# Optimization experiments

Measured on AMD Instinct MI355X. Metric: run time of the kernel, lower is better.

Reference implementation:

```python
import jax, jax.numpy as jnp
import numpy as np

N_NODES = 50000
N_GRAPHS = 500
E_SPARSE = 800000
E_DENSE = 3200000
IN_DIM = 128
HID = 128          # nb_hidden
OUT = HID // 2     # per-branch GATConv output
N_LAYERS = 3
NEG_SLOPE = 0.2    # PyG GATConv default


def setup_inputs() -> dict:
    key = jax.random.key(0)
    ks = jax.random.split(key, 10)
    x = jax.random.normal(ks[0], (N_NODES, IN_DIM), dtype=jnp.float32)
    edge_index = jax.random.randint(ks[1], (2, E_SPARSE), 0, N_NODES, dtype=jnp.int32)
    dense_edge_idx = jax.random.randint(ks[2], (2, E_DENSE), 0, N_NODES, dtype=jnp.int32)
    batch = jnp.sort(jax.random.randint(ks[3], (N_NODES,), 0, N_GRAPHS, dtype=jnp.int32))
    # One weight set per layer (source code aliases layersB = layersA, so both
    # branches share weights). All layers have in_dim = 128 -> out = 64.
    lin_w = jax.random.normal(ks[4], (N_LAYERS, HID, OUT), dtype=jnp.float32) * 0.1
    att_src = jax.random.normal(ks[5], (N_LAYERS, OUT), dtype=jnp.float32) * 0.1
    att_dst = jax.random.normal(ks[6], (N_LAYERS, OUT), dtype=jnp.float32) * 0.1
    bias = jnp.zeros((N_LAYERS, OUT), dtype=jnp.float32)
    final_w = jax.random.normal(ks[7], (HID, 1), dtype=jnp.float32) * 0.1
    final_b = jnp.zeros((1,), dtype=jnp.float32)
    return {"x": x, "edge_index": edge_index, "dense_edge_idx": dense_edge_idx,
            "batch": batch, "lin_w": lin_w, "att_src": att_src,
            "att_dst": att_dst, "bias": bias, "final_w": final_w,
            "final_b": final_b}


def _with_self_loops(edge_index, n):
    loop = jnp.arange(n, dtype=edge_index.dtype)
    src = jnp.concatenate([edge_index[0], loop])
    dst = jnp.concatenate([edge_index[1], loop])
    return src, dst


def _gat(x, src, dst, W, a_s, a_d, b):
    """PyG GATConv, heads=1: gather, LeakyReLU attention, segment softmax over
    incoming edges of each dst node, scatter-add aggregation."""
    n = x.shape[0]
    h = x @ W                      # [N, OUT]
    s_src = h @ a_s                # [N] per-node source score
    s_dst = h @ a_d                # [N] per-node dest score
    e = jax.nn.leaky_relu(s_src[src] + s_dst[dst], NEG_SLOPE)  # [E]
    m = jax.ops.segment_max(e, dst, num_segments=n)
    p = jnp.exp(e - m[dst])
    z = jax.ops.segment_sum(p, dst, num_segments=n)
    alpha = p / z[dst]             # [E] softmax over neighbors of dst
    out = jax.ops.segment_sum(alpha[:, None] * h[src], dst, num_segments=n)
    return out + b


def reference(x, edge_index, dense_edge_idx, batch, lin_w, att_src, att_dst,
              bias, final_w, final_b):
    n = x.shape[0]
    srcA, dstA = _with_self_loops(edge_index, n)
    srcB, dstB = _with_self_loops(dense_edge_idx, n)
    for l in range(N_LAYERS):
        xA = _gat(x, srcA, dstA, lin_w[l], att_src[l], att_dst[l], bias[l])
        xB = _gat(x, srcB, dstB, lin_w[l], att_src[l], att_dst[l], bias[l])
        x = jax.nn.relu(jnp.concatenate([xA, xB], axis=1))
    g = jax.ops.segment_sum(x, batch, num_segments=N_GRAPHS)  # global_add_pool
    y = (g @ final_w + final_b).squeeze()
    return y
```

## Files before the change

### kernel.cpp

```cpp
#include <hip/hip_runtime.h>
#include <hip/hip_fp16.h>

#define N_NODES 50000
#define N_GRAPHS 500
#define E_SPARSE 800000
#define E_DENSE 3200000
#define IN_DIM 128
#define HID 128
#define OUT_D 64
#define N_LAYERS 3
#define NEG_SLOPE 0.2f

#define BUCKET_SHIFT 7
#define BUCKET_N 128
#define NBUCK 391
#define NTD 256
#define NTS 64
#define TS_D 12500
#define TS_S 12500
#define MD (NBUCK * NTD)
#define MATN (NBUCK * (NTD + NTS))
#define NT 32
typedef unsigned int u32;
typedef unsigned short u16;
typedef _Float16 h16x8 __attribute__((ext_vector_type(8)));


__global__ __launch_bounds__(256) void tile_count_all(
    const int* __restrict__ dstD, const int* __restrict__ dstS,
    int* __restrict__ mat) {
    __shared__ int hc[NBUCK];
    int t = threadIdx.x;
    int tile = blockIdx.x;
    for (int i = t; i < NBUCK; i += 256) hc[i] = 0;
    __syncthreads();
    if (tile < NTD) {
        int beg = tile * TS_D, end = min(E_DENSE, beg + TS_D);
        for (int i = beg + t; i < end; i += 256)
            atomicAdd(&hc[dstD[i] >> BUCKET_SHIFT], 1);
        __syncthreads();
        for (int i = t; i < NBUCK; i += 256) mat[i * NTD + tile] = hc[i];
    } else {
        int st = tile - NTD;
        int beg = st * TS_S, end = min(E_SPARSE, beg + TS_S);
        for (int i = beg + t; i < end; i += 256)
            atomicAdd(&hc[dstS[i] >> BUCKET_SHIFT], 1);
        __syncthreads();
        for (int i = t; i < NBUCK; i += 256) mat[MD + i * NTS + st] = hc[i];
    }
}

__global__ void scan_lvl0(const int* __restrict__ cnt, int n,
                          int* __restrict__ out, int* __restrict__ bsum) {
    __shared__ int sm[512];
    int t = threadIdx.x;
    int base = blockIdx.x * 2048 + t * 4;
    int v0 = (base + 0 < n) ? cnt[base + 0] : 0;
    int v1 = (base + 1 < n) ? cnt[base + 1] : 0;
    int v2 = (base + 2 < n) ? cnt[base + 2] : 0;
    int v3 = (base + 3 < n) ? cnt[base + 3] : 0;
    int s = v0 + v1 + v2 + v3;
    sm[t] = s;
    __syncthreads();
    for (int off = 1; off < 512; off <<= 1) {
        int a = (t >= off) ? sm[t - off] : 0;
        __syncthreads();
        sm[t] += a;
        __syncthreads();
    }
    int excl = sm[t] - s;
    if (base + 0 < n) out[base + 0] = excl;
    if (base + 1 < n) out[base + 1] = excl + v0;
    if (base + 2 < n) out[base + 2] = excl + v0 + v1;
    if (base + 3 < n) out[base + 3] = excl + v0 + v1 + v2;
    if (t == 511) bsum[blockIdx.x] = sm[511];
}

__global__ void scan_lvl1(const int* __restrict__ bsum, int nb,
                          int* __restrict__ bsumx) {
    __shared__ int sm[256];
    int t = threadIdx.x;
    int v = (t < nb) ? bsum[t] : 0;
    sm[t] = v;
    __syncthreads();
    for (int off = 1; off < 256; off <<= 1) {
        int a = (t >= off) ? sm[t - off] : 0;
        __syncthreads();
        sm[t] += a;
        __syncthreads();
    }
    if (t < nb) bsumx[t] = sm[t] - v;
}

__global__ void scan_add(int* __restrict__ out, int n, const int* __restrict__ bsumx,
                         int Etot) {
    int i = blockIdx.x * blockDim.x + threadIdx.x;
    if (i < n) out[i] += bsumx[i >> 11];
    if (i == 0) out[n] = Etot;
}

__global__ __launch_bounds__(256) void tile_scatter_all(
    const int* __restrict__ srcD, const int* __restrict__ dstD,
    const int* __restrict__ srcS, const int* __restrict__ dstS,
    const int* __restrict__ matx, u32* __restrict__ pairs) {
    __shared__ int cur[NBUCK];
    int t = threadIdx.x;
    int tile = blockIdx.x;
    const int* src;
    const int* dst;
    int beg, end;
    if (tile < NTD) {
        for (int i = t; i < NBUCK; i += 256) cur[i] = matx[i * NTD + tile];
        src = srcD; dst = dstD;
        beg = tile * TS_D; end = min(E_DENSE, beg + TS_D);
    } else {
        int st = tile - NTD;
        for (int i = t; i < NBUCK; i += 256) cur[i] = matx[MD + i * NTS + st];
        src = srcS; dst = dstS;
        beg = st * TS_S; end = min(E_SPARSE, beg + TS_S);
    }
    __syncthreads();
    for (int i = beg + t; i < end; i += 256) {
        int d = dst[i];
        int pos = atomicAdd(&cur[d >> BUCKET_SHIFT], 1);
        pairs[pos] = (u32)src[i] | ((u32)(d & (BUCKET_N - 1)) << 16);
    }
}

__global__ __launch_bounds__(256) void bucket_to_csr_all(
    const u32* __restrict__ pairs, const int* __restrict__ matx,
    int* __restrict__ rowD, u16* __restrict__ csrcD,
    int* __restrict__ rowS, u16* __restrict__ csrcS) {
    int bid = blockIdx.x;
    int t = threadIdx.x;
    int b, beg, end, base;
    int* rowptr;
    u16* csrc;
    if (bid < NBUCK) {
        b = bid;
        beg = matx[b * NTD];
        end = matx[(b + 1) * NTD];
        base = 0; rowptr = rowD; csrc = csrcD;
    } else {
        b = bid - NBUCK;
        beg = matx[MD + b * NTS];
        end = matx[MD + (b + 1) * NTS];
        base = E_DENSE; rowptr = rowS; csrc = csrcS;
    }
    __shared__ int lcnt[BUCKET_N];
    __shared__ int lofs[BUCKET_N];
    if (t < BUCKET_N) lcnt[t] = 0;
    __syncthreads();
    for (int k = beg + t; k < end; k += 256)
        atomicAdd(&lcnt[(pairs[k] >> 16) & (BUCKET_N - 1)], 1);
    __syncthreads();
    if (t < BUCKET_N) lofs[t] = lcnt[t];
    __syncthreads();
    for (int off = 1; off < BUCKET_N; off <<= 1) {
        int a = (t < BUCKET_N && t >= off) ? lofs[t - off] : 0;
        __syncthreads();
        if (t < BUCKET_N) lofs[t] += a;
        __syncthreads();
    }
    int node = (b << BUCKET_SHIFT) + t;
    int lbeg = beg - base;
    if (t < BUCKET_N) {
        int excl = lofs[t] - lcnt[t];
        if (node < N_NODES) rowptr[node] = lbeg + excl;
        lcnt[t] = excl;
    }
    if (b == NBUCK - 1 && t == 0)
        rowptr[N_NODES] = (base == 0) ? E_DENSE : E_SPARSE;
    __syncthreads();
    for (int k = beg + t; k < end; k += 256) {
        u32 pr = pairs[k];
        int dl = (pr >> 16) & (BUCKET_N - 1);
        int pos = atomicAdd(&lcnt[dl], 1);
        csrc[lbeg + pos] = (u16)(pr & 0xffffu);
    }
}


__global__ __launch_bounds__(256) void node_mm2(
    const float* __restrict__ x, const float* __restrict__ W,
    const float* __restrict__ a_s, const float* __restrict__ a_d,
    __half* __restrict__ h, float* __restrict__ s_src, float* __restrict__ s_dst) {
    __shared__ float Wl[IN_DIM * OUT_D];
    __shared__ float4 Xl4[NT * 33];
    int t = threadIdx.x;
    int nbase = blockIdx.x * NT;

    const float4* W4 = (const float4*)W;
    float4* Wl4 = (float4*)Wl;
#pragma unroll
    for (int i = 0; i < 8; ++i) Wl4[t + 256 * i] = W4[t + 256 * i];

    int nrows = min(NT, N_NODES - nbase);
    const float4* X4 = (const float4*)(x + (size_t)nbase * IN_DIM);
    for (int i = t; i < nrows * 32; i += 256)
        Xl4[(i >> 5) * 33 + (i & 31)] = X4[i];
    __syncthreads();

    int wv = t >> 6, l = t & 63;
    int c4 = l & 15;
    int np = l >> 4;
    int n0 = wv * 8 + np * 2, n1 = n0 + 1;
    const float* Xl = (const float*)Xl4;
    const float4* Wr = (const float4*)Wl;

    float4 A0 = make_float4(0.f, 0.f, 0.f, 0.f);
    float4 A1 = make_float4(0.f, 0.f, 0.f, 0.f);
#pragma unroll 4
    for (int k = 0; k < IN_DIM; ++k) {
        float4 w4 = Wr[k * 16 + c4];
        float x0 = Xl[n0 * 132 + k];
        float x1 = Xl[n1 * 132 + k];
        A0.x += x0 * w4.x; A0.y += x0 * w4.y; A0.z += x0 * w4.z; A0.w += x0 * w4.w;
        A1.x += x1 * w4.x; A1.y += x1 * w4.y; A1.z += x1 * w4.z; A1.w += x1 * w4.w;
    }
    int gn0 = nbase + n0, gn1 = nbase + n1;
    if (gn0 < N_NODES) {
        __half2 v0 = __floats2half2_rn(A0.x, A0.y);
        __half2 v1 = __floats2half2_rn(A0.z, A0.w);
        float2 pk;
        pk.x = *(float*)&v0; pk.y = *(float*)&v1;
        ((float2*)(h + (size_t)gn0 * OUT_D))[c4] = pk;
    }
    if (gn1 < N_NODES) {
        __half2 v0 = __floats2half2_rn(A1.x, A1.y);
        __half2 v1 = __floats2half2_rn(A1.z, A1.w);
        float2 pk;
        pk.x = *(float*)&v0; pk.y = *(float*)&v1;
        ((float2*)(h + (size_t)gn1 * OUT_D))[c4] = pk;
    }

    float4 as4 = ((const float4*)a_s)[c4];
    float4 ad4 = ((const float4*)a_d)[c4];
    float ps0 = A0.x * as4.x + A0.y * as4.y + A0.z * as4.z + A0.w * as4.w;
    float pd0 = A0.x * ad4.x + A0.y * ad4.y + A0.z * ad4.z + A0.w * ad4.w;
    float ps1 = A1.x * as4.x + A1.y * as4.y + A1.z * as4.z + A1.w * as4.w;
    float pd1 = A1.x * ad4.x + A1.y * ad4.y + A1.z * ad4.z + A1.w * ad4.w;
#pragma unroll
    for (int off = 1; off < 16; off <<= 1) {
        ps0 += __shfl_xor(ps0, off); pd0 += __shfl_xor(pd0, off);
        ps1 += __shfl_xor(ps1, off); pd1 += __shfl_xor(pd1, off);
    }
    if (c4 == 0) {
        if (gn0 < N_NODES) { s_src[gn0] = ps0; s_dst[gn0] = pd0; }
        if (gn1 < N_NODES) { s_src[gn1] = ps1; s_dst[gn1] = pd1; }
    }
}

__device__ __forceinline__ void accv(float4& a0, float4& a1, float p,
                                     const h16x8& r) {
    a0.x = fmaf((float)r[0], p, a0.x);
    a0.y = fmaf((float)r[1], p, a0.y);
    a0.z = fmaf((float)r[2], p, a0.z);
    a0.w = fmaf((float)r[3], p, a0.w);
    a1.x = fmaf((float)r[4], p, a1.x);
    a1.y = fmaf((float)r[5], p, a1.y);
    a1.z = fmaf((float)r[6], p, a1.z);
    a1.w = fmaf((float)r[7], p, a1.w);
}

__device__ __forceinline__ float lrelu(float e) {
    return fmaxf(e, NEG_SLOPE * e);
}

__global__ __launch_bounds__(256, 8) void gat_aggr3(
    const int* __restrict__ rowS, const u16* __restrict__ csrcS,
    const int* __restrict__ rowD, const u16* __restrict__ csrcD,
    const float* __restrict__ s_src, const float* __restrict__ s_dst,
    const __half* __restrict__ h, const float* __restrict__ bias,
    float* __restrict__ xnext, int nblk) {
    int bid = blockIdx.x;
    const int* rowptr;
    const u16* csrc;
    int col_off;
    if (bid < nblk) { rowptr = rowS; csrc = csrcS; col_off = 0; }
    else { bid -= nblk; rowptr = rowD; csrc = csrcD; col_off = OUT_D; }

    int lane = threadIdx.x & 63;
    int wid = threadIdx.x >> 6;
    int grp = lane >> 3;
    int sub = lane & 7;
    int node = bid * 32 + wid * 8 + grp;
    bool valid = node < N_NODES;

    int beg = 0, end = 0;
    if (valid) { beg = rowptr[node]; end = rowptr[node + 1]; }
    float sd = valid ? s_dst[node] : 0.f;

    const char* hb = (const char*)h;
    u32 subo = (u32)sub * 16u;

    float4 a0 = make_float4(0.f, 0.f, 0.f, 0.f);
    float4 a1 = make_float4(0.f, 0.f, 0.f, 0.f);
    float z = 0.f;

    int k = beg;
    for (; k + 1 < end; k += 2) {
        u32 s0 = csrc[k], s1 = csrc[k + 1];
        h16x8 r0 = *(const h16x8*)(hb + (s0 * 128u + subo));
        h16x8 r1 = *(const h16x8*)(hb + (s1 * 128u + subo));
        float e0 = s_src[s0] + sd;
        float e1 = s_src[s1] + sd;
        float p0 = __expf(lrelu(e0));
        float p1 = __expf(lrelu(e1));
        z += p0 + p1;
        accv(a0, a1, p0, r0);
        accv(a0, a1, p1, r1);
    }
    if (k < end) {
        u32 s0 = csrc[k];
        h16x8 r0 = *(const h16x8*)(hb + (s0 * 128u + subo));
        float e0 = s_src[s0] + sd;
        float p0 = __expf(lrelu(e0));
        z += p0;
        accv(a0, a1, p0, r0);
    }
    if (valid) {
        h16x8 r0 = *(const h16x8*)(hb + ((u32)node * 128u + subo));
        float e0 = s_src[node] + sd;
        float p0 = __expf(lrelu(e0));
        z += p0;
        accv(a0, a1, p0, r0);

        float inv = 1.f / z;
        const float4* b4 = (const float4*)bias;
        float4 b0 = b4[sub * 2], b1 = b4[sub * 2 + 1];
        float4 o0, o1;
        o0.x = a0.x * inv + b0.x; o0.y = a0.y * inv + b0.y;
        o0.z = a0.z * inv + b0.z; o0.w = a0.w * inv + b0.w;
        o1.x = a1.x * inv + b1.x; o1.y = a1.y * inv + b1.y;
        o1.z = a1.z * inv + b1.z; o1.w = a1.w * inv + b1.w;
        o0.x = fmaxf(o0.x, 0.f); o0.y = fmaxf(o0.y, 0.f);
        o0.z = fmaxf(o0.z, 0.f); o0.w = fmaxf(o0.w, 0.f);
        o1.x = fmaxf(o1.x, 0.f); o1.y = fmaxf(o1.y, 0.f);
        o1.z = fmaxf(o1.z, 0.f); o1.w = fmaxf(o1.w, 0.f);
        float4* outp = (float4*)(xnext + (size_t)node * HID + col_off);
        outp[sub * 2] = o0;
        outp[sub * 2 + 1] = o1;
    }
}

__global__ __launch_bounds__(128) void pool_final(
    const float* __restrict__ x, const int* __restrict__ batch,
    const float* __restrict__ fw, const float* __restrict__ fb,
    float* __restrict__ y) {
    int b = blockIdx.x;
    int t = threadIdx.x;
    __shared__ int sbeg, send;
    if (t == 0) {
        int lo = 0, hi = N_NODES;
        while (lo < hi) { int mid = (lo + hi) >> 1; if (batch[mid] < b) lo = mid + 1; else hi = mid; }
        sbeg = lo;
        hi = N_NODES;
        while (lo < hi) { int mid = (lo + hi) >> 1; if (batch[mid] < b + 1) lo = mid + 1; else hi = mid; }
        send = lo;
    }
    __syncthreads();
    float acc = 0.f;
    for (int n = sbeg; n < send; ++n) acc += x[(size_t)n * HID + t];
    __shared__ float sm[HID];
    sm[t] = acc * fw[t];
    __syncthreads();
    for (int off = 64; off > 0; off >>= 1) {
        if (t < off) sm[t] += sm[t + off];
        __syncthreads();
    }
    if (t == 0) y[b] = sm[0] + fb[0];
}

extern "C" void kernel_launch(void* const* d_in, const int* in_sizes, int n_in,
                              void* d_out, int out_size, void* d_ws, size_t ws_size,
                              hipStream_t stream) {
    const float* x_in    = (const float*)d_in[0];
    const int*   ei      = (const int*)d_in[1];
    const int*   di      = (const int*)d_in[2];
    const int*   batch   = (const int*)d_in[3];
    const float* lin_w   = (const float*)d_in[4];
    const float* att_src = (const float*)d_in[5];
    const float* att_dst = (const float*)d_in[6];
    const float* bias    = (const float*)d_in[7];
    const float* fw      = (const float*)d_in[8];
    const float* fb      = (const float*)d_in[9];
    float* y = (float*)d_out;

    char* wsb = (char*)d_ws;
    size_t off = 0;
    auto alloc_b = [&](size_t bytes) { void* p = (void*)(wsb + off);
                                       off += (bytes + 15) & ~(size_t)15; return p; };

    float* xbuf0 = (float*)alloc_b((size_t)N_NODES * HID * 4);
    float* xbuf1 = (float*)alloc_b((size_t)N_NODES * HID * 4);
    __half* h    = (__half*)alloc_b((size_t)N_NODES * OUT_D * 2);
    float* s_src = (float*)alloc_b(N_NODES * 4);
    float* s_dst = (float*)alloc_b(N_NODES * 4);
    int* mat     = (int*)alloc_b((size_t)MATN * 4);
    int* matx    = (int*)alloc_b(((size_t)MATN + 1) * 4);
    int* bsum    = (int*)alloc_b(256 * 4);
    int* bsumx   = (int*)alloc_b(256 * 4);
    int* rowS    = (int*)alloc_b((N_NODES + 1) * 4);
    int* rowD    = (int*)alloc_b((N_NODES + 1) * 4);
    u16* csrcS   = (u16*)alloc_b((size_t)E_SPARSE * 2);
    u16* csrcD   = (u16*)alloc_b((size_t)E_DENSE * 2);
    u32* pairs   = (u32*)xbuf1;

    const int* srcD = di;
    const int* dstD = di + E_DENSE;
    const int* srcS = ei;
    const int* dstS = ei + E_SPARSE;

    const int SCAN_BLKS = (MATN + 2047) / 2048;

    tile_count_all<<<NTD + NTS, 256, 0, stream>>>(dstD, dstS, mat);
    scan_lvl0<<<SCAN_BLKS, 512, 0, stream>>>(mat, MATN, matx, bsum);
    scan_lvl1<<<1, 256, 0, stream>>>(bsum, SCAN_BLKS, bsumx);
    scan_add<<<(MATN + 256) / 256, 256, 0, stream>>>(matx, MATN, bsumx,
                                                     E_DENSE + E_SPARSE);
    tile_scatter_all<<<NTD + NTS, 256, 0, stream>>>(srcD, dstD, srcS, dstS,
                                                    matx, pairs);
    bucket_to_csr_all<<<2 * NBUCK, 256, 0, stream>>>(pairs, matx, rowD, csrcD,
                                                     rowS, csrcS);

    const float* cur = x_in;
    float* bufs[3] = {xbuf1, xbuf0, xbuf1};
    const int nblk = (N_NODES + 31) / 32;
    const int mm_grid = (N_NODES + NT - 1) / NT;
    for (int l = 0; l < N_LAYERS; ++l) {
        node_mm2<<<mm_grid, 256, 0, stream>>>(cur, lin_w + (size_t)l * HID * OUT_D,
                                              att_src + l * OUT_D, att_dst + l * OUT_D,
                                              h, s_src, s_dst);
        float* xn = bufs[l];
        gat_aggr3<<<2 * nblk, 256, 0, stream>>>(rowS, csrcS, rowD, csrcD,
                                                s_src, s_dst, h,
                                                bias + l * OUT_D, xn, nblk);
        cur = xn;
    }

    pool_final<<<N_GRAPHS, 128, 0, stream>>>(cur, batch, fw, fb, y);
}
```

Baseline: 511.4 us.

## Split feature gather into column halves with separate softmax-normalizer pass

```diff
diff --git a/kernel.cpp b/kernel.cpp
--- a/kernel.cpp
+++ b/kernel.cpp
@@ -8,6 +8,7 @@
 #define IN_DIM 128
 #define HID 128
 #define OUT_D 64
+#define OUT_H 32
 #define N_LAYERS 3
 #define NEG_SLOPE 0.2f
 
@@ -184,7 +185,8 @@
 __global__ __launch_bounds__(256) void node_mm2(
     const float* __restrict__ x, const float* __restrict__ W,
     const float* __restrict__ a_s, const float* __restrict__ a_d,
-    __half* __restrict__ h, float* __restrict__ s_src, float* __restrict__ s_dst) {
+    __half* __restrict__ h_lo, __half* __restrict__ h_hi,
+    float* __restrict__ s_src, float* __restrict__ s_dst) {
     __shared__ float Wl[IN_DIM * OUT_D];
     __shared__ float4 Xl4[NT * 33];
     int t = threadIdx.x;
@@ -219,19 +221,21 @@
         A1.x += x1 * w4.x; A1.y += x1 * w4.y; A1.z += x1 * w4.z; A1.w += x1 * w4.w;
     }
     int gn0 = nbase + n0, gn1 = nbase + n1;
+    __half* hdst = (c4 < 8) ? h_lo : h_hi;
+    int c4h = c4 & 7;
     if (gn0 < N_NODES) {
         __half2 v0 = __floats2half2_rn(A0.x, A0.y);
         __half2 v1 = __floats2half2_rn(A0.z, A0.w);
         float2 pk;
         pk.x = *(float*)&v0; pk.y = *(float*)&v1;
-        ((float2*)(h + (size_t)gn0 * OUT_D))[c4] = pk;
+        ((float2*)(hdst + (size_t)gn0 * OUT_H))[c4h] = pk;
     }
     if (gn1 < N_NODES) {
         __half2 v0 = __floats2half2_rn(A1.x, A1.y);
         __half2 v1 = __floats2half2_rn(A1.z, A1.w);
         float2 pk;
         pk.x = *(float*)&v0; pk.y = *(float*)&v1;
-        ((float2*)(h + (size_t)gn1 * OUT_D))[c4] = pk;
+        ((float2*)(hdst + (size_t)gn1 * OUT_H))[c4h] = pk;
     }
 
     float4 as4 = ((const float4*)a_s)[c4];
@@ -267,67 +271,101 @@
     return fmaxf(e, NEG_SLOPE * e);
 }
 
-__global__ __launch_bounds__(256, 8) void gat_aggr3(
+__global__ __launch_bounds__(256, 8) void gat_score(
     const int* __restrict__ rowS, const u16* __restrict__ csrcS,
     const int* __restrict__ rowD, const u16* __restrict__ csrcD,
     const float* __restrict__ s_src, const float* __restrict__ s_dst,
-    const __half* __restrict__ h, const float* __restrict__ bias,
-    float* __restrict__ xnext, int nblk) {
+    float* __restrict__ zinvS, float* __restrict__ zinvD, int ngrid) {
     int bid = blockIdx.x;
     const int* rowptr;
     const u16* csrc;
+    float* zinv;
+    if (bid < ngrid) { rowptr = rowS; csrc = csrcS; zinv = zinvS; }
+    else { bid -= ngrid; rowptr = rowD; csrc = csrcD; zinv = zinvD; }
+
+    int wid = threadIdx.x >> 6;
+    int lane = threadIdx.x & 63;
+    int node = bid * 4 + wid;
+    if (node >= N_NODES) return;
+
+    int beg = rowptr[node];
+    int end = rowptr[node + 1];
+    float sd = s_dst[node];
+
+    float z = 0.f;
+    for (int k = beg + lane; k < end; k += 64) {
+        u32 idx = csrc[k];
+        z += __expf(lrelu(s_src[idx] + sd));
+    }
+#pragma unroll
+    for (int off = 1; off <= 32; off <<= 1) z += __shfl_xor(z, off);
+    z += __expf(lrelu(s_src[node] + sd));
+    if (lane == 0) zinv[node] = 1.f / z;
+}
+
+__global__ __launch_bounds__(256, 8) void gat_gath(
+    const int* __restrict__ rowS, const u16* __restrict__ csrcS,
+    const float* __restrict__ zinvS,
+    const int* __restrict__ rowD, const u16* __restrict__ csrcD,
+    const float* __restrict__ zinvD,
+    const float* __restrict__ s_src, const float* __restrict__ s_dst,
+    const __half* __restrict__ hhalf, const float* __restrict__ biasH,
+    float* __restrict__ xnext, int ngrid, int halfoff) {
+    int bid = blockIdx.x;
+    const int* rowptr;
+    const u16* csrc;
+    const float* zinv;
     int col_off;
-    if (bid < nblk) { rowptr = rowS; csrc = csrcS; col_off = 0; }
-    else { bid -= nblk; rowptr = rowD; csrc = csrcD; col_off = OUT_D; }
-
+    if (bid < ngrid) { rowptr = rowS; csrc = csrcS; zinv = zinvS; col_off = halfoff; }
+    else { bid -= ngrid; rowptr = rowD; csrc = csrcD; zinv = zinvD; col_off = OUT_D + halfoff; }
+
+    int wid = threadIdx.x >> 6;
     int lane = threadIdx.x & 63;
-    int wid = threadIdx.x >> 6;
-    int grp = lane >> 3;
-    int sub = lane & 7;
-    int node = bid * 32 + wid * 8 + grp;
-    bool valid = node < N_NODES;
-
-    int beg = 0, end = 0;
-    if (valid) { beg = rowptr[node]; end = rowptr[node + 1]; }
-    float sd = valid ? s_dst[node] : 0.f;
-
-    const char* hb = (const char*)h;
+    int grp = lane >> 2;
+    int sub = lane & 3;
+    int node = bid * 4 + wid;
+    if (node >= N_NODES) return;
+
+    int beg = rowptr[node];
+    int end = rowptr[node + 1];
+    float sd = s_dst[node];
+
+    const char* hb = (const char*)hhalf;
     u32 subo = (u32)sub * 16u;
 
     float4 a0 = make_float4(0.f, 0.f, 0.f, 0.f);
     float4 a1 = make_float4(0.f, 0.f, 0.f, 0.f);
-    float z = 0.f;
-
-    int k = beg;
-    for (; k + 1 < end; k += 2) {
-        u32 s0 = csrc[k], s1 = csrc[k + 1];
-        h16x8 r0 = *(const h16x8*)(hb + (s0 * 128u + subo));
-        h16x8 r1 = *(const h16x8*)(hb + (s1 * 128u + subo));
-        float e0 = s_src[s0] + sd;
-        float e1 = s_src[s1] + sd;
-        float p0 = __expf(lrelu(e0));
-        float p1 = __expf(lrelu(e1));
-        z += p0 + p1;
+
+    int k = beg + grp;
+    for (; k + 16 < end; k += 32) {
+        u32 s0 = __builtin_nontemporal_load(&csrc[k]);
+        u32 s1 = __builtin_nontemporal_load(&csrc[k + 16]);
+        h16x8 r0 = *(const h16x8*)(hb + (s0 * 64u + subo));
+        h16x8 r1 = *(const h16x8*)(hb + (s1 * 64u + subo));
+        float p0 = __expf(lrelu(s_src[s0] + sd));
+        float p1 = __expf(lrelu(s_src[s1] + sd));
         accv(a0, a1, p0, r0);
         accv(a0, a1, p1, r1);
     }
     if (k < end) {
-        u32 s0 = csrc[k];
-        h16x8 r0 = *(const h16x8*)(hb + (s0 * 128u + subo));
-        float e0 = s_src[s0] + sd;
-        float p0 = __expf(lrelu(e0));
-        z += p0;
+        u32 s0 = __builtin_nontemporal_load(&csrc[k]);
+        h16x8 r0 = *(const h16x8*)(hb + (s0 * 64u + subo));
+        float p0 = __expf(lrelu(s_src[s0] + sd));
         accv(a0, a1, p0, r0);
     }
-    if (valid) {
-        h16x8 r0 = *(const h16x8*)(hb + ((u32)node * 128u + subo));
-        float e0 = s_src[node] + sd;
-        float p0 = __expf(lrelu(e0));
-        z += p0;
-        accv(a0, a1, p0, r0);
-
-        float inv = 1.f / z;
-        const float4* b4 = (const float4*)bias;
+#pragma unroll
+    for (int off = 4; off <= 32; off <<= 1) {
+        a0.x += __shfl_xor(a0.x, off); a0.y += __shfl_xor(a0.y, off);
+        a0.z += __shfl_xor(a0.z, off); a0.w += __shfl_xor(a0.w, off);
+        a1.x += __shfl_xor(a1.x, off); a1.y += __shfl_xor(a1.y, off);
+        a1.z += __shfl_xor(a1.z, off); a1.w += __shfl_xor(a1.w, off);
+    }
+    if (grp == 0) {
+        h16x8 rs = *(const h16x8*)(hb + ((u32)node * 64u + subo));
+        float ps = __expf(lrelu(s_src[node] + sd));
+        accv(a0, a1, ps, rs);
+        float inv = zinv[node];
+        const float4* b4 = (const float4*)biasH;
         float4 b0 = b4[sub * 2], b1 = b4[sub * 2 + 1];
         float4 o0, o1;
         o0.x = a0.x * inv + b0.x; o0.y = a0.y * inv + b0.y;
@@ -394,9 +432,12 @@
 
     float* xbuf0 = (float*)alloc_b((size_t)N_NODES * HID * 4);
     float* xbuf1 = (float*)alloc_b((size_t)N_NODES * HID * 4);
-    __half* h    = (__half*)alloc_b((size_t)N_NODES * OUT_D * 2);
+    __half* h_lo = (__half*)alloc_b((size_t)N_NODES * OUT_H * 2);
+    __half* h_hi = (__half*)alloc_b((size_t)N_NODES * OUT_H * 2);
     float* s_src = (float*)alloc_b(N_NODES * 4);
     float* s_dst = (float*)alloc_b(N_NODES * 4);
+    float* zinvS = (float*)alloc_b(N_NODES * 4);
+    float* zinvD = (float*)alloc_b(N_NODES * 4);
     int* mat     = (int*)alloc_b((size_t)MATN * 4);
     int* matx    = (int*)alloc_b(((size_t)MATN + 1) * 4);
     int* bsum    = (int*)alloc_b(256 * 4);
@@ -426,16 +467,25 @@
 
     const float* cur = x_in;
     float* bufs[3] = {xbuf1, xbuf0, xbuf1};
-    const int nblk = (N_NODES + 31) / 32;
+    const int ngrid = (N_NODES + 3) / 4;
     const int mm_grid = (N_NODES + NT - 1) / NT;
     for (int l = 0; l < N_LAYERS; ++l) {
         node_mm2<<<mm_grid, 256, 0, stream>>>(cur, lin_w + (size_t)l * HID * OUT_D,
                                               att_src + l * OUT_D, att_dst + l * OUT_D,
-                                              h, s_src, s_dst);
+                                              h_lo, h_hi, s_src, s_dst);
+        gat_score<<<2 * ngrid, 256, 0, stream>>>(rowS, csrcS, rowD, csrcD,
+                                                 s_src, s_dst, zinvS, zinvD,
+                                                 ngrid);
         float* xn = bufs[l];
-        gat_aggr3<<<2 * nblk, 256, 0, stream>>>(rowS, csrcS, rowD, csrcD,
-                                                s_src, s_dst, h,
-                                                bias + l * OUT_D, xn, nblk);
+        gat_gath<<<2 * ngrid, 256, 0, stream>>>(rowS, csrcS, zinvS,
+                                                rowD, csrcD, zinvD,
+                                                s_src, s_dst, h_lo,
+                                                bias + l * OUT_D, xn, ngrid, 0);
+        gat_gath<<<2 * ngrid, 256, 0, stream>>>(rowS, csrcS, zinvS,
+                                                rowD, csrcD, zinvD,
+                                                s_src, s_dst, h_hi,
+                                                bias + l * OUT_D + OUT_H,
+                                                xn, ngrid, OUT_H);
         cur = xn;
     }
 
```

Result: slower. 771.7 us (+50.9%).
